# Performance work log

Measured on AMD Instinct MI355X. Metric: run time of the kernel, lower is better.

Reference implementation:

```python
import jax, jax.numpy as jnp
import numpy as np

N = 100000
E = 1600000
IN_C = 128
HID = 128
NUM_CLASSES = 16


def setup_inputs() -> dict:
    key = jax.random.key(0)
    ks = jax.random.split(key, 8)
    x = jax.random.normal(ks[0], (N, IN_C), dtype=jnp.float32)
    edge_index = jax.random.randint(ks[1], (2, E), 0, N, dtype=jnp.int64)
    s1 = 1.0 / np.sqrt(IN_C)
    s2 = 1.0 / np.sqrt(HID)
    W1 = jax.random.uniform(ks[2], (IN_C, HID), jnp.float32, -s1, s1)
    b1 = jnp.zeros((HID,), jnp.float32)
    W2 = jax.random.uniform(ks[3], (HID, HID), jnp.float32, -s2, s2)
    b2 = jnp.zeros((HID,), jnp.float32)
    Wl = jax.random.uniform(ks[4], (HID, NUM_CLASSES), jnp.float32, -s2, s2)
    bl = jax.random.uniform(ks[5], (NUM_CLASSES,), jnp.float32, -s2, s2)
    return {"x": x, "edge_index": edge_index, "W1": W1, "b1": b1,
            "W2": W2, "b2": b2, "Wl": Wl, "bl": bl}


def gcn_conv(x, src, dst, norm, W, b, n_nodes):
    # x: [N, F_in]; src/dst: [E+N] (self-loops appended); norm: [E+N]
    h = x @ W  # [N, F_out] -- transform first (F_out <= F_in style), then gather
    msg = h[src] * norm[:, None]  # [E+N, F_out] gathered, normalized messages
    out = jax.ops.segment_sum(msg, dst, num_segments=n_nodes)  # scatter-add
    return out + b


def reference(x, edge_index, W1, b1, W2, b2, Wl, bl):
    loop = jnp.arange(N, dtype=edge_index.dtype)
    src = jnp.concatenate([edge_index[0], loop])  # add self-loops
    dst = jnp.concatenate([edge_index[1], loop])
    # symmetric GCN normalization: deg computed on target side incl. self-loops
    deg = jax.ops.segment_sum(jnp.ones_like(dst, dtype=x.dtype), dst,
                              num_segments=N)
    dinv = jnp.where(deg > 0, jax.lax.rsqrt(deg), 0.0)
    norm = dinv[src] * dinv[dst]  # [E+N]

    h = jax.nn.relu(gcn_conv(x, src, dst, norm, W1, b1, N))
    h = jax.nn.relu(gcn_conv(h, src, dst, norm, W2, b2, N))
    logits = h @ Wl + bl
    return jax.nn.softmax(logits, axis=1)
```

## Files before the change

kernel.cpp:

```cpp
#include <hip/hip_runtime.h>
#include <hip/hip_fp16.h>

#define FDIM 128
#define NCLS 16

#define SCAN_T 256
#define SCAN_I 8
#define SCAN_CHUNK (SCAN_T * SCAN_I)

typedef _Float16 f16x8 __attribute__((ext_vector_type(8)));
typedef float f32x4 __attribute__((ext_vector_type(4)));

__global__ void k_count(const int* __restrict__ dst, int* cnt, int e) {
    int i = blockIdx.x * blockDim.x + threadIdx.x;
    if (i < e) atomicAdd(&cnt[dst[i]], 1);
}

__global__ __launch_bounds__(SCAN_T) void k_scan1(const int* __restrict__ cnt,
                                                  int* __restrict__ excl,
                                                  int* __restrict__ blockSum,
                                                  float* __restrict__ dinv, int n) {
    __shared__ int ts[SCAN_T];
    int b = blockIdx.x, t = threadIdx.x;
    int base = b * SCAN_CHUNK + t * SCAN_I;
    int v[SCAN_I];
    int s = 0;
    #pragma unroll
    for (int i = 0; i < SCAN_I; ++i) {
        int idx = base + i;
        v[i] = (idx < n) ? cnt[idx] : 0;
        if (idx < n) dinv[idx] = rsqrtf((float)(v[i] + 1));
        s += v[i];
    }
    ts[t] = s;
    __syncthreads();
    for (int off = 1; off < SCAN_T; off <<= 1) {
        int x = (t >= off) ? ts[t - off] : 0;
        __syncthreads();
        ts[t] += x;
        __syncthreads();
    }
    int ex = (t == 0) ? 0 : ts[t - 1];
    #pragma unroll
    for (int i = 0; i < SCAN_I; ++i) {
        int idx = base + i;
        if (idx < n) excl[idx] = ex;
        ex += v[i];
    }
    if (t == SCAN_T - 1) blockSum[b] = ts[SCAN_T - 1];
}

__global__ __launch_bounds__(1024) void k_scan2(int* blockSum, int* total, int nb) {
    __shared__ int ts[1024];
    int t = threadIdx.x;
    int v = (t < nb) ? blockSum[t] : 0;
    ts[t] = v;
    __syncthreads();
    for (int off = 1; off < 1024; off <<= 1) {
        int x = (t >= off) ? ts[t - off] : 0;
        __syncthreads();
        ts[t] += x;
        __syncthreads();
    }
    if (t < nb) blockSum[t] = (t == 0) ? 0 : ts[t - 1];
    if (t == 1023) *total = ts[1023];
}

__global__ void k_scan3(int* __restrict__ row_ptr, int* __restrict__ cursor,
                        const int* __restrict__ blockSum, const int* __restrict__ total,
                        int n) {
    int i = blockIdx.x * blockDim.x + threadIdx.x;
    if (i < n) {
        int v = row_ptr[i] + blockSum[i / SCAN_CHUNK];
        row_ptr[i] = v;
        cursor[i] = v;
    }
    if (i == 0) row_ptr[n] = *total;
}

__global__ void k_scatter(const int* __restrict__ src, const int* __restrict__ dst,
                          int* cursor, int* __restrict__ csr_off, int e) {
    int i = blockIdx.x * blockDim.x + threadIdx.x;
    if (i >= e) return;
    int pos = atomicAdd(&cursor[dst[i]], 1);
    csr_off[pos] = src[i] << 8;
}

template <typename T>
__global__ __launch_bounds__(256) void k_gemm_mfma(const T* __restrict__ A,
                                                   const float* __restrict__ W,
                                                   const float* __restrict__ dinv,
                                                   __half* __restrict__ C, int n) {
    __shared__ _Float16 as[64 * 128];
    __shared__ _Float16 wt[128 * 128];
    int t = threadIdx.x;
    int r0 = blockIdx.x * 64;

    for (int i = t; i < 128 * 32; i += 256) {
        int k = i >> 5, c4 = (i & 31) * 4;
        float4 w4 = reinterpret_cast<const float4*>(W)[i];
        #pragma unroll
        for (int j = 0; j < 4; ++j) {
            int c = c4 + j;
            float wv = (j == 0) ? w4.x : (j == 1) ? w4.y : (j == 2) ? w4.z : w4.w;
            int byte = (c * 256 + k * 2) ^ ((c & 7) << 4);
            wt[byte >> 1] = (_Float16)wv;
        }
    }

    if constexpr (sizeof(T) == 4) {
        for (int i = t; i < 64 * 16; i += 256) {
            int r = i >> 4, c8 = i & 15;
            float4 v0 = make_float4(0.f, 0.f, 0.f, 0.f);
            float4 v1 = make_float4(0.f, 0.f, 0.f, 0.f);
            if (r0 + r < n) {
                v0 = reinterpret_cast<const float4*>(A)[(size_t)(r0 + r) * 32 + c8 * 2];
                v1 = reinterpret_cast<const float4*>(A)[(size_t)(r0 + r) * 32 + c8 * 2 + 1];
            }
            __half2 h0 = __float22half2_rn(make_float2(v0.x, v0.y));
            __half2 h1 = __float22half2_rn(make_float2(v0.z, v0.w));
            __half2 h2 = __float22half2_rn(make_float2(v1.x, v1.y));
            __half2 h3 = __float22half2_rn(make_float2(v1.z, v1.w));
            uint4 u;
            u.x = *reinterpret_cast<unsigned int*>(&h0);
            u.y = *reinterpret_cast<unsigned int*>(&h1);
            u.z = *reinterpret_cast<unsigned int*>(&h2);
            u.w = *reinterpret_cast<unsigned int*>(&h3);
            int byte = (r * 256 + c8 * 16) ^ ((r & 7) << 4);
            *reinterpret_cast<uint4*>(reinterpret_cast<char*>(as) + byte) = u;
        }
    } else {
        for (int i = t; i < 64 * 16; i += 256) {
            int r = i >> 4, c8 = i & 15;
            uint4 u = make_uint4(0, 0, 0, 0);
            if (r0 + r < n)
                u = reinterpret_cast<const uint4*>(A)[(size_t)(r0 + r) * 16 + c8];
            int byte = (r * 256 + c8 * 16) ^ ((r & 7) << 4);
            *reinterpret_cast<uint4*>(reinterpret_cast<char*>(as) + byte) = u;
        }
    }
    __syncthreads();

    int w = t >> 6, l = t & 63;
    int lrow = l & 15, lk = l >> 4;
    int rw = w * 16;

    f16x8 afrag[4];
    #pragma unroll
    for (int ks = 0; ks < 4; ++ks) {
        int row = rw + lrow;
        int byte = (row * 256 + (ks * 4 + lk) * 16) ^ ((row & 7) << 4);
        afrag[ks] = *reinterpret_cast<const f16x8*>(reinterpret_cast<const char*>(as) + byte);
    }
    float dv[4];
    #pragma unroll
    for (int reg = 0; reg < 4; ++reg) {
        int rg = r0 + rw + lk * 4 + reg;
        dv[reg] = (rg < n) ? dinv[rg] : 0.f;
    }

    #pragma unroll
    for (int ct = 0; ct < 8; ++ct) {
        f32x4 acc = {0.f, 0.f, 0.f, 0.f};
        #pragma unroll
        for (int ks = 0; ks < 4; ++ks) {
            int c = ct * 16 + lrow;
            int byte = (c * 256 + (ks * 4 + lk) * 16) ^ ((c & 7) << 4);
            f16x8 bfrag = *reinterpret_cast<const f16x8*>(reinterpret_cast<const char*>(wt) + byte);
            acc = __builtin_amdgcn_mfma_f32_16x16x32_f16(afrag[ks], bfrag, acc, 0, 0, 0);
        }
        #pragma unroll
        for (int reg = 0; reg < 4; ++reg) {
            int rg = r0 + rw + lk * 4 + reg;
            if (rg < n)
                C[(size_t)rg * FDIM + ct * 16 + lrow] = __float2half(acc[reg] * dv[reg]);
        }
    }
}

template <bool FUSE>
__global__ __launch_bounds__(256) void k_agg(const __half* __restrict__ Y,
                                             const int* __restrict__ csr_off,
                                             const int* __restrict__ row_ptr,
                                             const float* __restrict__ dinv,
                                             const float* __restrict__ bias,
                                             const float* __restrict__ Wl,
                                             const float* __restrict__ bl,
                                             __half* __restrict__ hout,
                                             float* __restrict__ out, int n) {
    __shared__ float s_wl[NCLS * FDIM];
    __shared__ float s_bl[NCLS];
    if (FUSE) {
        for (int i = threadIdx.x; i < FDIM * NCLS / 4; i += 256) {
            int k = i >> 2, c4 = (i & 3) * 4;
            float4 v = reinterpret_cast<const float4*>(Wl)[i];
            s_wl[(c4 + 0) * FDIM + k] = v.x;
            s_wl[(c4 + 1) * FDIM + k] = v.y;
            s_wl[(c4 + 2) * FDIM + k] = v.z;
            s_wl[(c4 + 3) * FDIM + k] = v.w;
        }
        if (threadIdx.x < NCLS) s_bl[threadIdx.x] = bl[threadIdx.x];
        __syncthreads();
    }

    int node = blockIdx.x * 4 + (threadIdx.x >> 6);
    if (node >= n) return;
    int lane = threadIdx.x & 63;
    int lb = lane << 2;

    const char* Yb = reinterpret_cast<const char*>(Y);
    float2 acc = __half22float2(
        *reinterpret_cast<const __half2*>(Yb + ((size_t)node << 8) + lb));
    int beg = row_ptr[node], end = row_ptr[node + 1];

    for (int j0 = beg; j0 < end; j0 += 64) {
        int cnt = min(64, end - j0);
        int myoff = (j0 + lane < end) ? csr_off[j0 + lane] : 0;
        int k = 0;
        for (; k + 16 <= cnt; k += 16) {
            __half2 v[16];
            #pragma unroll
            for (int i = 0; i < 16; ++i) {
                int o = __builtin_amdgcn_readlane(myoff, k + i);
                v[i] = *reinterpret_cast<const __half2*>(Yb + o + lb);
            }
            __half2 a0 = __hadd2(__hadd2(__hadd2(v[0], v[1]), __hadd2(v[2], v[3])),
                                 __hadd2(__hadd2(v[4], v[5]), __hadd2(v[6], v[7])));
            __half2 a1 = __hadd2(__hadd2(__hadd2(v[8], v[9]), __hadd2(v[10], v[11])),
                                 __hadd2(__hadd2(v[12], v[13]), __hadd2(v[14], v[15])));
            float2 f0 = __half22float2(a0);
            float2 f1 = __half22float2(a1);
            acc.x += f0.x + f1.x;
            acc.y += f0.y + f1.y;
        }
        for (; k + 8 <= cnt; k += 8) {
            __half2 v[8];
            #pragma unroll
            for (int i = 0; i < 8; ++i) {
                int o = __builtin_amdgcn_readlane(myoff, k + i);
                v[i] = *reinterpret_cast<const __half2*>(Yb + o + lb);
            }
            __half2 a0 = __hadd2(__hadd2(__hadd2(v[0], v[1]), __hadd2(v[2], v[3])),
                                 __hadd2(__hadd2(v[4], v[5]), __hadd2(v[6], v[7])));
            float2 f0 = __half22float2(a0);
            acc.x += f0.x;
            acc.y += f0.y;
        }
        for (; k < cnt; ++k) {
            int o = __builtin_amdgcn_readlane(myoff, k);
            float2 f = __half22float2(*reinterpret_cast<const __half2*>(Yb + o + lb));
            acc.x += f.x;
            acc.y += f.y;
        }
    }

    float di = dinv[node];
    float2 b = reinterpret_cast<const float2*>(bias)[lane];
    float hx = fmaxf(acc.x * di + b.x, 0.f);
    float hy = fmaxf(acc.y * di + b.y, 0.f);

    if (!FUSE) {
        reinterpret_cast<__half2*>(hout)[(size_t)node * 64 + lane] =
            __float22half2_rn(make_float2(hx, hy));
    } else {
        float lg[NCLS];
        #pragma unroll
        for (int c = 0; c < NCLS; ++c) {
            float2 w2 = *reinterpret_cast<const float2*>(&s_wl[c * FDIM + lane * 2]);
            lg[c] = hx * w2.x + hy * w2.y;
        }
        #pragma unroll
        for (int off = 1; off < 64; off <<= 1) {
            #pragma unroll
            for (int c = 0; c < NCLS; ++c) lg[c] += __shfl_xor(lg[c], off, 64);
        }
        #pragma unroll
        for (int c = 0; c < NCLS; ++c) lg[c] += s_bl[c];
        float m = lg[0];
        #pragma unroll
        for (int c = 1; c < NCLS; ++c) m = fmaxf(m, lg[c]);
        float ev[NCLS];
        float sum = 0.f;
        #pragma unroll
        for (int c = 0; c < NCLS; ++c) { ev[c] = __expf(lg[c] - m); sum += ev[c]; }
        float inv = 1.0f / sum;
        float mye = 0.f;
        #pragma unroll
        for (int c = 0; c < NCLS; ++c) if (lane == c) mye = ev[c];
        if (lane < NCLS) out[(size_t)node * NCLS + lane] = mye * inv;
    }
}

extern "C" void kernel_launch(void* const* d_in, const int* in_sizes, int n_in,
                              void* d_out, int out_size, void* d_ws, size_t ws_size,
                              hipStream_t stream) {
    const float* x  = (const float*)d_in[0];
    const int*   ei = (const int*)d_in[1];
    const float* W1 = (const float*)d_in[2];
    const float* b1 = (const float*)d_in[3];
    const float* W2 = (const float*)d_in[4];
    const float* b2 = (const float*)d_in[5];
    const float* Wl = (const float*)d_in[6];
    const float* bl = (const float*)d_in[7];
    float* out = (float*)d_out;

    int n = in_sizes[0] / FDIM;
    int e = in_sizes[1] / 2;
    const int* src = ei;
    const int* dst = ei + e;

    int nb = (n + SCAN_CHUNK - 1) / SCAN_CHUNK;

    float* dinv    = (float*)d_ws;
    int*   cnt     = (int*)(dinv + n);
    int*   row_ptr = cnt + n;
    int*   cursor  = row_ptr + n + 1;
    int*   blockSum= cursor + n;
    int*   total   = blockSum + 1024;
    int*   csr_off = total + 1;
    uintptr_t p = (uintptr_t)(csr_off + e);
    p = (p + 15) & ~(uintptr_t)15;
    __half* bufA = (__half*)p;
    __half* bufB = bufA + (size_t)n * FDIM;

    int bn = (n + 255) / 256;
    int be = (e + 255) / 256;

    hipMemsetAsync(cnt, 0, (size_t)n * sizeof(int), stream);
    k_count<<<be, 256, 0, stream>>>(dst, cnt, e);
    k_scan1<<<nb, SCAN_T, 0, stream>>>(cnt, row_ptr, blockSum, dinv, n);
    k_scan2<<<1, 1024, 0, stream>>>(blockSum, total, nb);
    k_scan3<<<bn, 256, 0, stream>>>(row_ptr, cursor, blockSum, total, n);
    k_scatter<<<be, 256, 0, stream>>>(src, dst, cursor, csr_off, e);

    int bg = (n + 63) / 64;
    int ba = (n + 3) / 4;

    k_gemm_mfma<float><<<bg, 256, 0, stream>>>(x, W1, dinv, bufA, n);
    k_agg<false><<<ba, 256, 0, stream>>>(bufA, csr_off, row_ptr, dinv, b1, Wl, bl, bufB, out, n);

    k_gemm_mfma<__half><<<bg, 256, 0, stream>>>(bufB, W2, dinv, bufA, n);
    k_agg<true><<<ba, 256, 0, stream>>>(bufA, csr_off, row_ptr, dinv, b2, Wl, bl, bufB, out, n);
}
```

Baseline: 509.3 us.

## Pretranspose weights to fp16, enlarge GEMM tiles, split-lane layer-1 aggregation

```diff
diff --git a/kernel.cpp b/kernel.cpp
--- a/kernel.cpp
+++ b/kernel.cpp
@@ -86,30 +86,47 @@
     csr_off[pos] = src[i] << 8;
 }
 
+__global__ __launch_bounds__(256) void k_prepw(const float* __restrict__ W1,
+                                               const float* __restrict__ W2,
+                                               __half* __restrict__ T1,
+                                               __half* __restrict__ T2) {
+    const float* W = (blockIdx.x == 0) ? W1 : W2;
+    __half* T = (blockIdx.x == 0) ? T1 : T2;
+    int t = threadIdx.x;
+    for (int i = t; i < 128 * 32; i += 256) {
+        int c = i >> 5, k4 = (i & 31) * 4;
+        float a = W[(k4 + 0) * 128 + c];
+        float b = W[(k4 + 1) * 128 + c];
+        float d = W[(k4 + 2) * 128 + c];
+        float f = W[(k4 + 3) * 128 + c];
+        __half2 h0 = __float22half2_rn(make_float2(a, b));
+        __half2 h1 = __float22half2_rn(make_float2(d, f));
+        uint2 u;
+        u.x = *reinterpret_cast<unsigned int*>(&h0);
+        u.y = *reinterpret_cast<unsigned int*>(&h1);
+        *reinterpret_cast<uint2*>(&T[c * 128 + k4]) = u;
+    }
+}
+
 template <typename T>
-__global__ __launch_bounds__(256) void k_gemm_mfma(const T* __restrict__ A,
-                                                   const float* __restrict__ W,
+__global__ __launch_bounds__(512) void k_gemm_mfma(const T* __restrict__ A,
+                                                   const __half* __restrict__ WT,
                                                    const float* __restrict__ dinv,
                                                    __half* __restrict__ C, int n) {
-    __shared__ _Float16 as[64 * 128];
+    __shared__ _Float16 as[128 * 128];
     __shared__ _Float16 wt[128 * 128];
     int t = threadIdx.x;
-    int r0 = blockIdx.x * 64;
-
-    for (int i = t; i < 128 * 32; i += 256) {
-        int k = i >> 5, c4 = (i & 31) * 4;
-        float4 w4 = reinterpret_cast<const float4*>(W)[i];
-        #pragma unroll
-        for (int j = 0; j < 4; ++j) {
-            int c = c4 + j;
-            float wv = (j == 0) ? w4.x : (j == 1) ? w4.y : (j == 2) ? w4.z : w4.w;
-            int byte = (c * 256 + k * 2) ^ ((c & 7) << 4);
-            wt[byte >> 1] = (_Float16)wv;
-        }
+    int r0 = blockIdx.x * 128;
+
+    for (int i = t; i < 2048; i += 512) {
+        int c = i >> 4, k8 = i & 15;
+        uint4 u = reinterpret_cast<const uint4*>(WT)[i];
+        int byte = (c * 256 + k8 * 16) ^ ((c & 7) << 4);
+        *reinterpret_cast<uint4*>(reinterpret_cast<char*>(wt) + byte) = u;
     }
 
     if constexpr (sizeof(T) == 4) {
-        for (int i = t; i < 64 * 16; i += 256) {
+        for (int i = t; i < 128 * 16; i += 512) {
             int r = i >> 4, c8 = i & 15;
             float4 v0 = make_float4(0.f, 0.f, 0.f, 0.f);
             float4 v1 = make_float4(0.f, 0.f, 0.f, 0.f);
@@ -130,7 +147,7 @@
             *reinterpret_cast<uint4*>(reinterpret_cast<char*>(as) + byte) = u;
         }
     } else {
-        for (int i = t; i < 64 * 16; i += 256) {
+        for (int i = t; i < 128 * 16; i += 512) {
             int r = i >> 4, c8 = i & 15;
             uint4 u = make_uint4(0, 0, 0, 0);
             if (r0 + r < n)
@@ -178,30 +195,105 @@
     }
 }
 
-template <bool FUSE>
-__global__ __launch_bounds__(256) void k_agg(const __half* __restrict__ Y,
-                                             const int* __restrict__ csr_off,
-                                             const int* __restrict__ row_ptr,
-                                             const float* __restrict__ dinv,
-                                             const float* __restrict__ bias,
-                                             const float* __restrict__ Wl,
-                                             const float* __restrict__ bl,
-                                             __half* __restrict__ hout,
-                                             float* __restrict__ out, int n) {
+__global__ __launch_bounds__(256) void k_agg_v2(const __half* __restrict__ Y,
+                                                const int* __restrict__ csr_off,
+                                                const int* __restrict__ row_ptr,
+                                                const float* __restrict__ dinv,
+                                                const float* __restrict__ bias,
+                                                __half* __restrict__ hout, int n) {
+    int node = blockIdx.x * 4 + (threadIdx.x >> 6);
+    if (node >= n) return;
+    int lane = threadIdx.x & 63;
+    int half = lane >> 5, l32 = lane & 31;
+    const char* Yb = reinterpret_cast<const char*>(Y);
+    const char* lanebase = Yb + (l32 << 3);
+
+    float a0 = 0.f, a1 = 0.f, a2 = 0.f, a3 = 0.f;
+    int beg = row_ptr[node], end = row_ptr[node + 1];
+
+    for (int j0 = beg; j0 < end; j0 += 64) {
+        int cnt = min(64, end - j0);
+        int myoff = (j0 + lane < end) ? csr_off[j0 + lane] : 0;
+        int k = 0;
+        for (; k + 8 <= cnt; k += 8) {
+            uint2 u[4];
+            #pragma unroll
+            for (int i = 0; i < 4; ++i) {
+                int oe = __builtin_amdgcn_readlane(myoff, k + 2 * i);
+                int oo = __builtin_amdgcn_readlane(myoff, k + 2 * i + 1);
+                int off = half ? oo : oe;
+                u[i] = *reinterpret_cast<const uint2*>(lanebase + off);
+            }
+            __half2* p = reinterpret_cast<__half2*>(u);
+            __half2 lo = __hadd2(__hadd2(p[0], p[2]), __hadd2(p[4], p[6]));
+            __half2 hi = __hadd2(__hadd2(p[1], p[3]), __hadd2(p[5], p[7]));
+            float2 flo = __half22float2(lo), fhi = __half22float2(hi);
+            a0 += flo.x; a1 += flo.y; a2 += fhi.x; a3 += fhi.y;
+        }
+        for (; k + 2 <= cnt; k += 2) {
+            int oe = __builtin_amdgcn_readlane(myoff, k);
+            int oo = __builtin_amdgcn_readlane(myoff, k + 1);
+            int off = half ? oo : oe;
+            uint2 u = *reinterpret_cast<const uint2*>(lanebase + off);
+            __half2* p = reinterpret_cast<__half2*>(&u);
+            float2 flo = __half22float2(p[0]), fhi = __half22float2(p[1]);
+            a0 += flo.x; a1 += flo.y; a2 += fhi.x; a3 += fhi.y;
+        }
+        if (k < cnt) {
+            int o = __builtin_amdgcn_readlane(myoff, k);
+            uint2 u = *reinterpret_cast<const uint2*>(lanebase + o);
+            __half2* p = reinterpret_cast<__half2*>(&u);
+            float sel = (half == 0) ? 1.0f : 0.0f;
+            float2 flo = __half22float2(p[0]), fhi = __half22float2(p[1]);
+            a0 += flo.x * sel; a1 += flo.y * sel;
+            a2 += fhi.x * sel; a3 += fhi.y * sel;
+        }
+    }
+
+    a0 += __shfl_xor(a0, 32, 64);
+    a1 += __shfl_xor(a1, 32, 64);
+    a2 += __shfl_xor(a2, 32, 64);
+    a3 += __shfl_xor(a3, 32, 64);
+
+    uint2 su = *reinterpret_cast<const uint2*>(Yb + ((size_t)node << 8) + (l32 << 3));
+    __half2* sp = reinterpret_cast<__half2*>(&su);
+    float2 slo = __half22float2(sp[0]), shi = __half22float2(sp[1]);
+    a0 += slo.x; a1 += slo.y; a2 += shi.x; a3 += shi.y;
+
+    float di = dinv[node];
+    float4 b = *reinterpret_cast<const float4*>(bias + l32 * 4);
+    __half2 h0 = __float22half2_rn(make_float2(fmaxf(a0 * di + b.x, 0.f),
+                                               fmaxf(a1 * di + b.y, 0.f)));
+    __half2 h1 = __float22half2_rn(make_float2(fmaxf(a2 * di + b.z, 0.f),
+                                               fmaxf(a3 * di + b.w, 0.f)));
+    if (half == 0) {
+        uint2 o;
+        o.x = *reinterpret_cast<unsigned int*>(&h0);
+        o.y = *reinterpret_cast<unsigned int*>(&h1);
+        *reinterpret_cast<uint2*>(reinterpret_cast<char*>(hout) + ((size_t)node << 8) + (l32 << 3)) = o;
+    }
+}
+
+__global__ __launch_bounds__(256) void k_agg_fuse(const __half* __restrict__ Y,
+                                                  const int* __restrict__ csr_off,
+                                                  const int* __restrict__ row_ptr,
+                                                  const float* __restrict__ dinv,
+                                                  const float* __restrict__ bias,
+                                                  const float* __restrict__ Wl,
+                                                  const float* __restrict__ bl,
+                                                  float* __restrict__ out, int n) {
     __shared__ float s_wl[NCLS * FDIM];
     __shared__ float s_bl[NCLS];
-    if (FUSE) {
-        for (int i = threadIdx.x; i < FDIM * NCLS / 4; i += 256) {
-            int k = i >> 2, c4 = (i & 3) * 4;
-            float4 v = reinterpret_cast<const float4*>(Wl)[i];
-            s_wl[(c4 + 0) * FDIM + k] = v.x;
-            s_wl[(c4 + 1) * FDIM + k] = v.y;
-            s_wl[(c4 + 2) * FDIM + k] = v.z;
-            s_wl[(c4 + 3) * FDIM + k] = v.w;
-        }
-        if (threadIdx.x < NCLS) s_bl[threadIdx.x] = bl[threadIdx.x];
-        __syncthreads();
-    }
+    for (int i = threadIdx.x; i < FDIM * NCLS / 4; i += 256) {
+        int k = i >> 2, c4 = (i & 3) * 4;
+        float4 v = reinterpret_cast<const float4*>(Wl)[i];
+        s_wl[(c4 + 0) * FDIM + k] = v.x;
+        s_wl[(c4 + 1) * FDIM + k] = v.y;
+        s_wl[(c4 + 2) * FDIM + k] = v.z;
+        s_wl[(c4 + 3) * FDIM + k] = v.w;
+    }
+    if (threadIdx.x < NCLS) s_bl[threadIdx.x] = bl[threadIdx.x];
+    __syncthreads();
 
     int node = blockIdx.x * 4 + (threadIdx.x >> 6);
     if (node >= n) return;
@@ -259,36 +351,31 @@
     float hx = fmaxf(acc.x * di + b.x, 0.f);
     float hy = fmaxf(acc.y * di + b.y, 0.f);
 
-    if (!FUSE) {
-        reinterpret_cast<__half2*>(hout)[(size_t)node * 64 + lane] =
-            __float22half2_rn(make_float2(hx, hy));
-    } else {
-        float lg[NCLS];
+    float lg[NCLS];
+    #pragma unroll
+    for (int c = 0; c < NCLS; ++c) {
+        float2 w2 = *reinterpret_cast<const float2*>(&s_wl[c * FDIM + lane * 2]);
+        lg[c] = hx * w2.x + hy * w2.y;
+    }
+    #pragma unroll
+    for (int off = 1; off < 64; off <<= 1) {
         #pragma unroll
-        for (int c = 0; c < NCLS; ++c) {
-            float2 w2 = *reinterpret_cast<const float2*>(&s_wl[c * FDIM + lane * 2]);
-            lg[c] = hx * w2.x + hy * w2.y;
-        }
-        #pragma unroll
-        for (int off = 1; off < 64; off <<= 1) {
-            #pragma unroll
-            for (int c = 0; c < NCLS; ++c) lg[c] += __shfl_xor(lg[c], off, 64);
-        }
-        #pragma unroll
-        for (int c = 0; c < NCLS; ++c) lg[c] += s_bl[c];
-        float m = lg[0];
-        #pragma unroll
-        for (int c = 1; c < NCLS; ++c) m = fmaxf(m, lg[c]);
-        float ev[NCLS];
-        float sum = 0.f;
-        #pragma unroll
-        for (int c = 0; c < NCLS; ++c) { ev[c] = __expf(lg[c] - m); sum += ev[c]; }
-        float inv = 1.0f / sum;
-        float mye = 0.f;
-        #pragma unroll
-        for (int c = 0; c < NCLS; ++c) if (lane == c) mye = ev[c];
-        if (lane < NCLS) out[(size_t)node * NCLS + lane] = mye * inv;
-    }
+        for (int c = 0; c < NCLS; ++c) lg[c] += __shfl_xor(lg[c], off, 64);
+    }
+    #pragma unroll
+    for (int c = 0; c < NCLS; ++c) lg[c] += s_bl[c];
+    float m = lg[0];
+    #pragma unroll
+    for (int c = 1; c < NCLS; ++c) m = fmaxf(m, lg[c]);
+    float ev[NCLS];
+    float sum = 0.f;
+    #pragma unroll
+    for (int c = 0; c < NCLS; ++c) { ev[c] = __expf(lg[c] - m); sum += ev[c]; }
+    float inv = 1.0f / sum;
+    float mye = 0.f;
+    #pragma unroll
+    for (int c = 0; c < NCLS; ++c) if (lane == c) mye = ev[c];
+    if (lane < NCLS) out[(size_t)node * NCLS + lane] = mye * inv;
 }
 
 extern "C" void kernel_launch(void* const* d_in, const int* in_sizes, int n_in,
@@ -320,25 +407,28 @@
     int*   csr_off = total + 1;
     uintptr_t p = (uintptr_t)(csr_off + e);
     p = (p + 15) & ~(uintptr_t)15;
-    __half* bufA = (__half*)p;
+    __half* wt1 = (__half*)p;
+    __half* wt2 = wt1 + 128 * 128;
+    __half* bufA = wt2 + 128 * 128;
     __half* bufB = bufA + (size_t)n * FDIM;
 
     int bn = (n + 255) / 256;
     int be = (e + 255) / 256;
 
     hipMemsetAsync(cnt, 0, (size_t)n * sizeof(int), stream);
+    k_prepw<<<2, 256, 0, stream>>>(W1, W2, wt1, wt2);
     k_count<<<be, 256, 0, stream>>>(dst, cnt, e);
     k_scan1<<<nb, SCAN_T, 0, stream>>>(cnt, row_ptr, blockSum, dinv, n);
     k_scan2<<<1, 1024, 0, stream>>>(blockSum, total, nb);
     k_scan3<<<bn, 256, 0, stream>>>(row_ptr, cursor, blockSum, total, n);
     k_scatter<<<be, 256, 0, stream>>>(src, dst, cursor, csr_off, e);
 
-    int bg = (n + 63) / 64;
+    int bg = (n + 127) / 128;
     int ba = (n + 3) / 4;
 
-    k_gemm_mfma<float><<<bg, 256, 0, stream>>>(x, W1, dinv, bufA, n);
-    k_agg<false><<<ba, 256, 0, stream>>>(bufA, csr_off, row_ptr, dinv, b1, Wl, bl, bufB, out, n);
-
-    k_gemm_mfma<__half><<<bg, 256, 0, stream>>>(bufB, W2, dinv, bufA, n);
-    k_agg<true><<<ba, 256, 0, stream>>>(bufA, csr_off, row_ptr, dinv, b2, Wl, bl, bufB, out, n);
-}
+    k_gemm_mfma<float><<<bg, 512, 0, stream>>>(x, wt1, dinv, bufA, n);
+    k_agg_v2<<<ba, 256, 0, stream>>>(bufA, csr_off, row_ptr, dinv, b1, bufB, n);
+
+    k_gemm_mfma<__half><<<bg, 512, 0, stream>>>(bufB, wt2, dinv, bufA, n);
+    k_agg_fuse<<<ba, 256, 0, stream>>>(bufA, csr_off, row_ptr, dinv, b2, Wl, bl, out, n);
+}
```

After: 477.6 us. -6.2%, faster.
